# Performance work log

Measured on AMD Instinct MI355X. Metric: run time of the kernel, lower is better.

## Reference

```python
import jax, jax.numpy as jnp
import numpy as np

N, D, H, E = 50000, 128, 256, 400000


def setup_inputs() -> dict:
    key = jax.random.key(0)
    ks = jax.random.split(key, 10)
    s2d = 1.0 / np.sqrt(2 * D)
    sh = 1.0 / np.sqrt(H)
    return {
        "embeddings": jax.random.normal(ks[0], (N, D), jnp.float32),
        "edge_index": jax.random.randint(ks[1], (2, E), 0, N, jnp.int64),
        # contradiction_detector: Linear(2D,H) -> ReLU -> Linear(H,1) -> Sigmoid
        "Wd1": jax.random.uniform(ks[2], (2 * D, H), jnp.float32, -s2d, s2d),
        "bd1": jax.random.uniform(ks[3], (H,), jnp.float32, -s2d, s2d),
        "Wd2": jax.random.uniform(ks[4], (H, 1), jnp.float32, -sh, sh),
        "bd2": jax.random.uniform(ks[5], (1,), jnp.float32, -sh, sh),
        # resolver: Linear(2D,H) -> ReLU -> Linear(H,D)
        "Wr1": jax.random.uniform(ks[6], (2 * D, H), jnp.float32, -s2d, s2d),
        "br1": jax.random.uniform(ks[7], (H,), jnp.float32, -s2d, s2d),
        "Wr2": jax.random.uniform(ks[8], (H, D), jnp.float32, -sh, sh),
        "br2": jax.random.uniform(ks[9], (D,), jnp.float32, -sh, sh),
    }


def reference(embeddings, edge_index, Wd1, bd1, Wd2, bd2, Wr1, br1, Wr2, br2):
    src, dst = edge_index[0], edge_index[1]
    # gather src/dst features for every edge and concat: (E, 2D)
    pair = jnp.concatenate([embeddings[src], embeddings[dst]], axis=-1)
    # batched detector MLP -> per-edge contradiction score (E,)
    scores = jax.nn.sigmoid(jax.nn.relu(pair @ Wd1 + bd1) @ Wd2 + bd2)[:, 0]
    # batched resolver MLP (depends only on ORIGINAL embeddings): (E, D)
    resolution = jax.nn.relu(pair @ Wr1 + br1) @ Wr2 + br2
    mask = scores > 0.5
    n_edges = src.shape[0]
    n_nodes = embeddings.shape[0]
    # Sequential overwrite semantics: the LAST contradicting edge touching a
    order = jnp.where(mask, jnp.arange(1, n_edges + 1, dtype=jnp.int32), 0)
    last = jnp.zeros((n_nodes,), jnp.int32).at[src].max(order).at[dst].max(order)
    idx = jnp.maximum(last - 1, 0)
    resolved = jnp.where((last > 0)[:, None],
                         (embeddings + resolution[idx]) * 0.5,
                         embeddings)
    return resolved, scores
```

## Files before the change

### kernel.cpp

```cpp
#include <hip/hip_runtime.h>
#include <math.h>

#define NN 50000
#define DD 128
#define K2D 256
#define HH 256
#define EE 400000
#define TE 64
#define RT 32
#define PST 260
#define TAU  0.005f
#define TAU2 5e-5f
#define DGRID 512

typedef __attribute__((ext_vector_type(8))) short bf16x8;
typedef __attribute__((ext_vector_type(4))) float f32x4;
typedef unsigned int uint;
typedef unsigned short ushort;

typedef __attribute__((address_space(3))) void lds_void_t;
typedef __attribute__((address_space(1))) void g1_void_t;

__device__ __forceinline__ ushort f2bf(float x) {
    uint u = __builtin_bit_cast(uint, x);
    u = (u + 0x7FFFu + ((u >> 16) & 1u)) >> 16;
    return (ushort)u;
}

__device__ __forceinline__ int stageOff(int r, int k) {
    return ((r >> 4) * 8 + (k >> 5)) * 512 + ((((k >> 3) & 3) << 4) + (r & 15)) * 8 + (k & 7);
}

__device__ __forceinline__ void swz_unit(const float* __restrict__ W,
                                         ushort* __restrict__ out,
                                         int N, int Kt, int unit, int l)
{
    const int n = unit / Kt, t = unit - n * Kt;
    const int row0 = t * 32 + (l >> 4) * 8;
    const int col = n * 16 + (l & 15);
    ushort tmp[8];
#pragma unroll
    for (int j = 0; j < 8; ++j) tmp[j] = f2bf(W[(row0 + j) * N + col]);
    uint4 p;
    p.x = (uint)tmp[0] | ((uint)tmp[1] << 16);
    p.y = (uint)tmp[2] | ((uint)tmp[3] << 16);
    p.z = (uint)tmp[4] | ((uint)tmp[5] << 16);
    p.w = (uint)tmp[6] | ((uint)tmp[7] << 16);
    *(uint4*)(out + ((size_t)unit * 64 + l) * 8) = p;
}

__global__ __launch_bounds__(256) void prep_kernel(
    const float* __restrict__ emb, ushort* __restrict__ embbf, int doConv,
    const float* __restrict__ Wd1, ushort* __restrict__ wd1s,
    const float* __restrict__ Wr1, ushort* __restrict__ wr1s,
    const float* __restrict__ Wr2, ushort* __restrict__ wr2s)
{
    const int gid = blockIdx.x;
    const int tid = threadIdx.x;
    if (gid < 3125) {
        if (!doConv) return;
        const int i = gid * 256 + tid;
        const float4 a = ((const float4*)emb)[(size_t)i * 2];
        const float4 b = ((const float4*)emb)[(size_t)i * 2 + 1];
        uint4 p;
        p.x = (uint)f2bf(a.x) | ((uint)f2bf(a.y) << 16);
        p.y = (uint)f2bf(a.z) | ((uint)f2bf(a.w) << 16);
        p.z = (uint)f2bf(b.x) | ((uint)f2bf(b.y) << 16);
        p.w = (uint)f2bf(b.z) | ((uint)f2bf(b.w) << 16);
        *(uint4*)(embbf + (size_t)i * 8) = p;
        return;
    }
    const int sub = tid >> 6, l = tid & 63;
    if (gid < 3125 + 32) {
        swz_unit(Wd1, wd1s, HH, 8, (gid - 3125) * 4 + sub, l);
    } else if (gid < 3125 + 64) {
        swz_unit(Wr1, wr1s, HH, 8, (gid - 3125 - 32) * 4 + sub, l);
    } else {
        swz_unit(Wr2, wr2s, DD, 8, (gid - 3125 - 64) * 4 + sub, l);
    }
}

__global__ __launch_bounds__(256) void det_pipe(
    const ushort* __restrict__ embbf,
    const int* __restrict__ srcIdx, const int* __restrict__ dstIdx,
    const ushort* __restrict__ w1s, const float* __restrict__ b1,
    const float* __restrict__ W2, const float* __restrict__ b2p,
    float* __restrict__ scores,
    int* __restrict__ last,
    int* __restrict__ flagCount, int* __restrict__ flagList, int flagCap)
{
    __shared__ __align__(16) ushort A[2][TE * K2D];
    __shared__ float zp[2][256];
    const int tid = threadIdx.x;
    const int wv = tid >> 6;
    const int lane = tid & 63;
    const int lc = lane & 15, lg = lane >> 4;
    const int nT = EE / TE;
    const int stride = gridDim.x;

    float b1v[4], w2v[4];
#pragma unroll
    for (int n = 0; n < 4; ++n) {
        const int col = wv * 64 + n * 16 + lc;
        b1v[n] = b1[col];
        w2v[n] = W2[col];
    }
    const float b2v = *b2p;
    const ushort* wbase = w1s + (size_t)(wv * 4) * 8 * 512;

    auto STAGE = [&](int T, int bp) {
        const int e = T * TE + wv * 16 + lc;
        const int ns = srcIdx[e], nd = dstIdx[e];
        const int ko = lg * 8;
#pragma unroll
        for (int s = 0; s < 8; ++s) {
            const int node = (s < 4) ? ns : nd;
            const ushort* g = embbf + (size_t)node * DD + (s & 3) * 32 + ko;
            __builtin_amdgcn_global_load_lds((const g1_void_t*)g,
                                             (lds_void_t*)&A[bp][(wv * 8 + s) * 512],
                                             16, 0, 0);
        }
    };

    int T = blockIdx.x;
    int cur = 0;
    STAGE(T, 0);

    for (; T < nT; T += stride) {
        const int Tn = T + stride;
        if (Tn < nT) {
            STAGE(Tn, cur ^ 1);
            asm volatile("s_waitcnt vmcnt(8)" ::: "memory");
        } else {
            asm volatile("s_waitcnt vmcnt(0)" ::: "memory");
        }
        __builtin_amdgcn_sched_barrier(0);
        __builtin_amdgcn_s_barrier();
        __builtin_amdgcn_sched_barrier(0);

        f32x4 acc[4][4] = {};
#pragma unroll 2
        for (int t = 0; t < 8; ++t) {
            bf16x8 af[4], bfr[4];
#pragma unroll
            for (int m = 0; m < 4; ++m)
                af[m] = *(const bf16x8*)&A[cur][(m * 8 + t) * 512 + lane * 8];
#pragma unroll
            for (int n = 0; n < 4; ++n)
                bfr[n] = *(const bf16x8*)(wbase + (n * 8 + t) * 512 + lane * 8);
#pragma unroll
            for (int m = 0; m < 4; ++m)
#pragma unroll
                for (int n = 0; n < 4; ++n)
                    acc[m][n] = __builtin_amdgcn_mfma_f32_16x16x32_bf16(af[m], bfr[n], acc[m][n], 0, 0, 0);
        }

        float pz[4][4];
#pragma unroll
        for (int m = 0; m < 4; ++m)
#pragma unroll
            for (int r = 0; r < 4; ++r) {
                float s = 0.f;
#pragma unroll
                for (int n = 0; n < 4; ++n)
                    s = fmaf(fmaxf(acc[m][n][r] + b1v[n], 0.f), w2v[n], s);
                pz[m][r] = s;
            }
#pragma unroll
        for (int msk = 1; msk <= 8; msk <<= 1)
#pragma unroll
            for (int m = 0; m < 4; ++m)
#pragma unroll
                for (int r = 0; r < 4; ++r)
                    pz[m][r] += __shfl_xor(pz[m][r], msk, 64);
        if (lc == 0) {
#pragma unroll
            for (int m = 0; m < 4; ++m)
#pragma unroll
                for (int r = 0; r < 4; ++r)
                    zp[cur][wv * 64 + m * 16 + lg * 4 + r] = pz[m][r];
        }

        asm volatile("s_waitcnt lgkmcnt(0)" ::: "memory");
        __builtin_amdgcn_sched_barrier(0);
        __builtin_amdgcn_s_barrier();
        __builtin_amdgcn_sched_barrier(0);

        if (tid < 64) {
            const int e = T * TE + tid;
            const float z = zp[cur][tid] + zp[cur][64 + tid] +
                            zp[cur][128 + tid] + zp[cur][192 + tid] + b2v;
            scores[e] = 1.0f / (1.0f + expf(-z));
            bool deferred = false;
            if (fabsf(z) < TAU) {
                const int slot = atomicAdd(flagCount, 1);
                if (slot < flagCap) { flagList[slot] = e; deferred = true; }
            }
            if (!deferred && z > 0.0f) {
                atomicMax(&last[srcIdx[e]], e + 1);
                atomicMax(&last[dstIdx[e]], e + 1);
            }
        }
        cur ^= 1;
    }
}

__global__ __launch_bounds__(256) void det_kernel(
    const float* __restrict__ emb,
    const int* __restrict__ srcIdx, const int* __restrict__ dstIdx,
    const ushort* __restrict__ w1s, const float* __restrict__ b1,
    const float* __restrict__ W2, const float* __restrict__ b2p,
    float* __restrict__ scores,
    int* __restrict__ last,
    int* __restrict__ flagCount, int* __restrict__ flagList, int flagCap)
{
    __shared__ __align__(16) ushort A_lds[TE * K2D];
    __shared__ float zp[256];
    const int tid = threadIdx.x;
    const int e0 = blockIdx.x * TE;
    {
        const int r = tid >> 2, q = tid & 3;
        const int e = e0 + r;
        const int node = (q < 2) ? srcIdx[e] : dstIdx[e];
        const float4* s4 = (const float4*)(emb + (size_t)node * DD + (q & 1) * 64);
#pragma unroll
        for (int u = 0; u < 16; ++u) {
            const float4 v = s4[u];
            const int k0 = q * 64 + u * 4;
            uint2 p;
            p.x = (uint)f2bf(v.x) | ((uint)f2bf(v.y) << 16);
            p.y = (uint)f2bf(v.z) | ((uint)f2bf(v.w) << 16);
            *(uint2*)&A_lds[stageOff(r, k0)] = p;
        }
    }
    __syncthreads();

    const int wv = tid >> 6;
    const int lane = tid & 63;
    const int lc = lane & 15, lg = lane >> 4;

    f32x4 acc[4][4] = {};
    const ushort* wbase = w1s + (size_t)(wv * 4) * 8 * 512;
#pragma unroll 2
    for (int t = 0; t < 8; ++t) {
        bf16x8 af[4], bfr[4];
#pragma unroll
        for (int m = 0; m < 4; ++m)
            af[m] = *(const bf16x8*)&A_lds[(m * 8 + t) * 512 + lane * 8];
#pragma unroll
        for (int n = 0; n < 4; ++n)
            bfr[n] = *(const bf16x8*)(wbase + (n * 8 + t) * 512 + lane * 8);
#pragma unroll
        for (int m = 0; m < 4; ++m)
#pragma unroll
            for (int n = 0; n < 4; ++n)
                acc[m][n] = __builtin_amdgcn_mfma_f32_16x16x32_bf16(af[m], bfr[n], acc[m][n], 0, 0, 0);
    }
    float b1v[4], w2v[4];
#pragma unroll
    for (int n = 0; n < 4; ++n) {
        const int col = wv * 64 + n * 16 + lc;
        b1v[n] = b1[col];
        w2v[n] = W2[col];
    }
    float pz[4][4];
#pragma unroll
    for (int m = 0; m < 4; ++m)
#pragma unroll
        for (int r = 0; r < 4; ++r) {
            float s = 0.f;
#pragma unroll
            for (int n = 0; n < 4; ++n)
                s = fmaf(fmaxf(acc[m][n][r] + b1v[n], 0.f), w2v[n], s);
            pz[m][r] = s;
        }
#pragma unroll
    for (int msk = 1; msk <= 8; msk <<= 1)
#pragma unroll
        for (int m = 0; m < 4; ++m)
#pragma unroll
            for (int r = 0; r < 4; ++r)
                pz[m][r] += __shfl_xor(pz[m][r], msk, 64);
    if (lc == 0) {
#pragma unroll
        for (int m = 0; m < 4; ++m)
#pragma unroll
            for (int r = 0; r < 4; ++r)
                zp[wv * 64 + m * 16 + lg * 4 + r] = pz[m][r];
    }
    __syncthreads();
    if (tid < 64) {
        const int e = e0 + tid;
        const float z = zp[tid] + zp[64 + tid] + zp[128 + tid] + zp[192 + tid] + *b2p;
        scores[e] = 1.0f / (1.0f + expf(-z));
        bool deferred = false;
        if (fabsf(z) < TAU) {
            const int slot = atomicAdd(flagCount, 1);
            if (slot < flagCap) { flagList[slot] = e; deferred = true; }
        }
        if (!deferred && z > 0.0f) {
            atomicMax(&last[srcIdx[e]], e + 1);
            atomicMax(&last[dstIdx[e]], e + 1);
        }
    }
}

__global__ __launch_bounds__(256) void refine_kernel(
    const float* __restrict__ emb,
    const int* __restrict__ srcIdx, const int* __restrict__ dstIdx,
    const float* __restrict__ W1, const float* __restrict__ b1,
    const float* __restrict__ W2, const float* __restrict__ b2p,
    int* __restrict__ last,
    const int* __restrict__ flagCount, const int* __restrict__ flagList,
    int flagCap)
{
    __shared__ __align__(16) float P[RT * PST];
    __shared__ int eL[RT];
    __shared__ float zs[RT];
    __shared__ int need64[RT];
    __shared__ double wsumd[4];
    const int tid = threadIdx.x;
    const int cnt = min(*flagCount, flagCap);
    const int nTiles = (cnt + RT - 1) / RT;
    const float b2v = *b2p;

    for (int T = blockIdx.x; T < nTiles; T += gridDim.x) {
        if (tid < RT) {
            const int idx = T * RT + tid;
            eL[tid] = flagList[min(idx, cnt - 1)];
            need64[tid] = 0;
        }
        __syncthreads();
        {
            const int i = tid >> 3, q = tid & 7;
            const int e = eL[i];
            const int node = (q < 4) ? srcIdx[e] : dstIdx[e];
            const float4* s4 = (const float4*)(emb + (size_t)node * DD + (q & 3) * 32);
            float4* d4 = (float4*)(P + i * PST + q * 32);
#pragma unroll
            for (int t = 0; t < 8; ++t) d4[t] = s4[t];
        }
        __syncthreads();

        const int rowg = tid >> 5;
        const int colg = tid & 31;
        const int c0 = colg * 8;

        float acc[4][8];
#pragma unroll
        for (int c = 0; c < 8; ++c) {
            const float bv = b1[c0 + c];
#pragma unroll
            for (int r = 0; r < 4; ++r) acc[r][c] = bv;
        }
        for (int kk = 0; kk < K2D; kk += 4) {
            float af[4][4];
#pragma unroll
            for (int r = 0; r < 4; ++r) {
                const float4 v = *(const float4*)&P[(rowg * 4 + r) * PST + kk];
                af[r][0] = v.x; af[r][1] = v.y; af[r][2] = v.z; af[r][3] = v.w;
            }
#pragma unroll
            for (int dk = 0; dk < 4; ++dk) {
                const float4 w0 = *(const float4*)&W1[(kk + dk) * HH + c0];
                const float4 w1 = *(const float4*)&W1[(kk + dk) * HH + c0 + 4];
#pragma unroll
                for (int r = 0; r < 4; ++r) {
                    const float av = af[r][dk];
                    acc[r][0] = fmaf(av, w0.x, acc[r][0]);
                    acc[r][1] = fmaf(av, w0.y, acc[r][1]);
                    acc[r][2] = fmaf(av, w0.z, acc[r][2]);
                    acc[r][3] = fmaf(av, w0.w, acc[r][3]);
                    acc[r][4] = fmaf(av, w1.x, acc[r][4]);
                    acc[r][5] = fmaf(av, w1.y, acc[r][5]);
                    acc[r][6] = fmaf(av, w1.z, acc[r][6]);
                    acc[r][7] = fmaf(av, w1.w, acc[r][7]);
                }
            }
        }

        float w2[8];
#pragma unroll
        for (int c = 0; c < 8; ++c) w2[c] = W2[c0 + c];
        float pz[4];
#pragma unroll
        for (int r = 0; r < 4; ++r) {
            float s = 0.f;
#pragma unroll
            for (int c = 0; c < 8; ++c) s = fmaf(fmaxf(acc[r][c], 0.f), w2[c], s);
            pz[r] = s;
        }
#pragma unroll
        for (int m = 1; m <= 16; m <<= 1) {
#pragma unroll
            for (int r = 0; r < 4; ++r) pz[r] += __shfl_xor(pz[r], m, 64);
        }
        if (colg == 0) {
#pragma unroll
            for (int r = 0; r < 4; ++r) zs[rowg * 4 + r] = pz[r] + b2v;
        }
        __syncthreads();

        if (tid < RT) {
            const int idx = T * RT + tid;
            if (idx < cnt) {
                const float z = zs[tid];
                if (fabsf(z) < TAU2) {
                    need64[tid] = 1;
                } else if (z > 0.f) {
                    const int e = eL[tid];
                    atomicMax(&last[srcIdx[e]], e + 1);
                    atomicMax(&last[dstIdx[e]], e + 1);
                }
            }
        }
        __syncthreads();

        for (int r = 0; r < RT; ++r) {
            if (!need64[r]) continue;
            const int j = tid;
            double h0 = 0.0, h1 = 0.0;
            for (int k = 0; k < K2D; k += 2) {
                h0 += (double)P[r * PST + k]     * (double)W1[(k)     * HH + j];
                h1 += (double)P[r * PST + k + 1] * (double)W1[(k + 1) * HH + j];
            }
            const double h = (double)b1[j] + h0 + h1;
            double v = (h > 0.0) ? h * (double)W2[j] : 0.0;
#pragma unroll
            for (int m = 1; m <= 32; m <<= 1) v += __shfl_xor(v, m, 64);
            if ((tid & 63) == 0) wsumd[tid >> 6] = v;
            __syncthreads();
            if (tid == 0) {
                const double z = wsumd[0] + wsumd[1] + wsumd[2] + wsumd[3] + (double)b2v;
                if (z > 0.0) {
                    const int e = eL[r];
                    atomicMax(&last[srcIdx[e]], e + 1);
                    atomicMax(&last[dstIdx[e]], e + 1);
                }
            }
            __syncthreads();
        }
        __syncthreads();
    }
}

template<int BF>
__global__ __launch_bounds__(256) void res_kernel(
    const float* __restrict__ emb, const ushort* __restrict__ embbf,
    const int* __restrict__ srcIdx, const int* __restrict__ dstIdx,
    const ushort* __restrict__ w1s, const float* __restrict__ b1,
    const ushort* __restrict__ w2s, const float* __restrict__ b2,
    const int* __restrict__ last,
    float* __restrict__ outRes)
{
    __shared__ __align__(16) ushort A_lds[TE * K2D];
    __shared__ int lastL[TE];
    const int tid = threadIdx.x;
    const int n0 = blockIdx.x * TE;
    const int wv = tid >> 6;
    const int lane = tid & 63;

    if (tid < TE) {
        const int n = n0 + tid;
        lastL[tid] = (n < NN) ? last[n] : 0;
    }
    if (BF) {
        const int r = wv * 16 + (lane & 15);
        const int n = n0 + r;
        int e = 0;
        if (n < NN) { const int lv = last[n]; if (lv > 0) e = lv - 1; }
        const int ns = srcIdx[e], nd = dstIdx[e];
        const int ko = (lane >> 4) * 8;
#pragma unroll
        for (int s = 0; s < 8; ++s) {
            const int node = (s < 4) ? ns : nd;
            const ushort* g = embbf + (size_t)node * DD + (s & 3) * 32 + ko;
            __builtin_amdgcn_global_load_lds((const g1_void_t*)g,
                                             (lds_void_t*)&A_lds[(wv * 8 + s) * 512],
                                             16, 0, 0);
        }
    } else {
        const int r = tid >> 2, q = tid & 3;
        const int n = n0 + r;
        int e = 0;
        if (n < NN) { const int l = last[n]; if (l > 0) e = l - 1; }
        const int node = (q < 2) ? srcIdx[e] : dstIdx[e];
        const float4* s4 = (const float4*)(emb + (size_t)node * DD + (q & 1) * 64);
#pragma unroll
        for (int u = 0; u < 16; ++u) {
            const float4 v = s4[u];
            const int k0 = q * 64 + u * 4;
            uint2 p;
            p.x = (uint)f2bf(v.x) | ((uint)f2bf(v.y) << 16);
            p.y = (uint)f2bf(v.z) | ((uint)f2bf(v.w) << 16);
            *(uint2*)&A_lds[stageOff(r, k0)] = p;
        }
    }
    __syncthreads();

    const int lc = lane & 15, lg = lane >> 4;

    f32x4 acc[4][4] = {};
    {
        const ushort* wbase = w1s + (size_t)(wv * 4) * 8 * 512;
#pragma unroll 2
        for (int t = 0; t < 8; ++t) {
            bf16x8 af[4], bfr[4];
#pragma unroll
            for (int m = 0; m < 4; ++m)
                af[m] = *(const bf16x8*)&A_lds[(m * 8 + t) * 512 + lane * 8];
#pragma unroll
            for (int n = 0; n < 4; ++n)
                bfr[n] = *(const bf16x8*)(wbase + (n * 8 + t) * 512 + lane * 8);
#pragma unroll
            for (int m = 0; m < 4; ++m)
#pragma unroll
                for (int n = 0; n < 4; ++n)
                    acc[m][n] = __builtin_amdgcn_mfma_f32_16x16x32_bf16(af[m], bfr[n], acc[m][n], 0, 0, 0);
        }
    }
    float b1v[4];
#pragma unroll
    for (int n = 0; n < 4; ++n) b1v[n] = b1[wv * 64 + n * 16 + lc];

    __syncthreads();
#pragma unroll
    for (int m = 0; m < 4; ++m)
#pragma unroll
        for (int n = 0; n < 4; ++n) {
            const int hcol = wv * 64 + n * 16 + lc;
#pragma unroll
            for (int r = 0; r < 4; ++r) {
                const int row = m * 16 + lg * 4 + r;
                A_lds[stageOff(row, hcol)] = f2bf(fmaxf(acc[m][n][r] + b1v[n], 0.f));
            }
        }
    __syncthreads();

    f32x4 acc2[4][2] = {};
    {
        const ushort* wbase = w2s + (size_t)(wv * 2) * 8 * 512;
#pragma unroll 2
        for (int t = 0; t < 8; ++t) {
            bf16x8 af[4], bfr[2];
#pragma unroll
            for (int m = 0; m < 4; ++m)
                af[m] = *(const bf16x8*)&A_lds[(m * 8 + t) * 512 + lane * 8];
#pragma unroll
            for (int n = 0; n < 2; ++n)
                bfr[n] = *(const bf16x8*)(wbase + (n * 8 + t) * 512 + lane * 8);
#pragma unroll
            for (int m = 0; m < 4; ++m)
#pragma unroll
                for (int n = 0; n < 2; ++n)
                    acc2[m][n] = __builtin_amdgcn_mfma_f32_16x16x32_bf16(af[m], bfr[n], acc2[m][n], 0, 0, 0);
        }
    }
    float b2v[2];
#pragma unroll
    for (int n = 0; n < 2; ++n) b2v[n] = b2[(wv * 2 + n) * 16 + lc];

#pragma unroll
    for (int m = 0; m < 4; ++m)
#pragma unroll
        for (int r = 0; r < 4; ++r) {
            const int row = m * 16 + lg * 4 + r;
            const int n = n0 + row;
            if (n >= NN) continue;
            const bool hit = lastL[row] > 0;
#pragma unroll
            for (int c = 0; c < 2; ++c) {
                const int col = (wv * 2 + c) * 16 + lc;
                const float ev = emb[(size_t)n * DD + col];
                outRes[(size_t)n * DD + col] =
                    hit ? (ev + acc2[m][c][r] + b2v[c]) * 0.5f : ev;
            }
        }
}

extern "C" void kernel_launch(void* const* d_in, const int* in_sizes, int n_in,
                              void* d_out, int out_size, void* d_ws, size_t ws_size,
                              hipStream_t stream)
{
    const float* emb = (const float*)d_in[0];
    const int*   edge = (const int*)d_in[1];
    const float* Wd1 = (const float*)d_in[2];
    const float* bd1 = (const float*)d_in[3];
    const float* Wd2 = (const float*)d_in[4];
    const float* bd2 = (const float*)d_in[5];
    const float* Wr1 = (const float*)d_in[6];
    const float* br1 = (const float*)d_in[7];
    const float* Wr2 = (const float*)d_in[8];
    const float* br2 = (const float*)d_in[9];

    const int* srcIdx = edge;
    const int* dstIdx = edge + EE;

    float* outRes = (float*)d_out;
    float* scores = outRes + (size_t)NN * DD;

    int* last = (int*)d_ws;
    int* flagCount = last + 50112;
    ushort* wd1s = (ushort*)(last + 50176);
    ushort* wr1s = wd1s + 65536;
    ushort* wr2s = wr1s + 65536;
    int* flagList = (int*)(wr2s + 32768);
    ushort* embbf = (ushort*)(flagList + 65536);

    const size_t base   = 50176u * 4 + (65536u + 65536u + 32768u) * 2 + 65536u * 4;
    const size_t needBF = base + (size_t)NN * DD * 2;
    const int useBF = (ws_size >= needBF) ? 1 : 0;

    int flagCap = 65536;
    if (ws_size < base) {
        long avail = ((long)ws_size - (long)(base - 65536u * 4)) / 4;
        flagCap = avail < 0 ? 0 : (int)avail;
    }

    hipMemsetAsync(d_ws, 0, 50176 * sizeof(int), stream);

    prep_kernel<<<3205, 256, 0, stream>>>(emb, embbf, useBF,
                                          Wd1, wd1s, Wr1, wr1s, Wr2, wr2s);

    if (useBF) {
        det_pipe<<<DGRID, 256, 0, stream>>>(embbf, srcIdx, dstIdx,
                                            wd1s, bd1, Wd2, bd2,
                                            scores, last, flagCount, flagList, flagCap);
    } else {
        det_kernel<<<EE / TE, 256, 0, stream>>>(emb, srcIdx, dstIdx,
                                                wd1s, bd1, Wd2, bd2,
                                                scores, last, flagCount, flagList, flagCap);
    }
    refine_kernel<<<1024, 256, 0, stream>>>(emb, srcIdx, dstIdx,
                                            Wd1, bd1, Wd2, bd2,
                                            last, flagCount, flagList, flagCap);
    if (useBF) {
        res_kernel<1><<<(NN + TE - 1) / TE, 256, 0, stream>>>(emb, embbf, srcIdx, dstIdx,
                                                              wr1s, br1, wr2s, br2,
                                                              last, outRes);
    } else {
        res_kernel<0><<<(NN + TE - 1) / TE, 256, 0, stream>>>(emb, embbf, srcIdx, dstIdx,
                                                              wr1s, br1, wr2s, br2,
                                                              last, outRes);
    }
}
```

Baseline: 194.0 us.

## Replace persistent LDS double-buffered detector with one-tile-per-block register-fed kernel

Swaps the persistent, double-buffered detector kernel, which staged gathered bf16 embeddings into LDS with global_load_lds, for a non-persistent kernel launched with one 64-edge tile per block. Each lane loads its A fragments directly from global memory into registers and feeds the MFMAs, so no LDS staging or cross-iteration barriers are needed. A launch_bounds occupancy hint of 3 is added. The intent is to rely on occupancy rather than explicit prefetch to hide gather latency, at the cost of many more block launches and no software pipelining.

```diff
diff --git a/kernel.cpp b/kernel.cpp
--- a/kernel.cpp
+++ b/kernel.cpp
@@ -11,7 +11,6 @@
 #define PST 260
 #define TAU  0.005f
 #define TAU2 5e-5f
-#define DGRID 512
 
 typedef __attribute__((ext_vector_type(8))) short bf16x8;
 typedef __attribute__((ext_vector_type(4))) float f32x4;
@@ -80,7 +79,7 @@
     }
 }
 
-__global__ __launch_bounds__(256) void det_pipe(
+__global__ __launch_bounds__(256, 3) void det_reg(
     const ushort* __restrict__ embbf,
     const int* __restrict__ srcIdx, const int* __restrict__ dstIdx,
     const ushort* __restrict__ w1s, const float* __restrict__ b1,
@@ -89,14 +88,39 @@
     int* __restrict__ last,
     int* __restrict__ flagCount, int* __restrict__ flagList, int flagCap)
 {
-    __shared__ __align__(16) ushort A[2][TE * K2D];
-    __shared__ float zp[2][256];
+    __shared__ float zp[256];
     const int tid = threadIdx.x;
+    const int e0 = blockIdx.x * TE;
     const int wv = tid >> 6;
     const int lane = tid & 63;
     const int lc = lane & 15, lg = lane >> 4;
-    const int nT = EE / TE;
-    const int stride = gridDim.x;
+
+    const ushort* baseS[4];
+    const ushort* baseD[4];
+#pragma unroll
+    for (int m = 0; m < 4; ++m) {
+        const int e = e0 + m * 16 + lc;
+        baseS[m] = embbf + (size_t)srcIdx[e] * DD + lg * 8;
+        baseD[m] = embbf + (size_t)dstIdx[e] * DD + lg * 8;
+    }
+    const ushort* wbase = w1s + (size_t)(wv * 4) * 8 * 512;
+
+    f32x4 acc[4][4] = {};
+#pragma unroll
+    for (int t = 0; t < 8; ++t) {
+        bf16x8 af[4], bfr[4];
+#pragma unroll
+        for (int m = 0; m < 4; ++m)
+            af[m] = *(const bf16x8*)(((t < 4) ? baseS[m] : baseD[m]) + (t & 3) * 32);
+#pragma unroll
+        for (int n = 0; n < 4; ++n)
+            bfr[n] = *(const bf16x8*)(wbase + (size_t)(n * 8 + t) * 512 + lane * 8);
+#pragma unroll
+        for (int m = 0; m < 4; ++m)
+#pragma unroll
+            for (int n = 0; n < 4; ++n)
+                acc[m][n] = __builtin_amdgcn_mfma_f32_16x16x32_bf16(af[m], bfr[n], acc[m][n], 0, 0, 0);
+    }
 
     float b1v[4], w2v[4];
 #pragma unroll
@@ -105,103 +129,46 @@
         b1v[n] = b1[col];
         w2v[n] = W2[col];
     }
-    const float b2v = *b2p;
-    const ushort* wbase = w1s + (size_t)(wv * 4) * 8 * 512;
-
-    auto STAGE = [&](int T, int bp) {
-        const int e = T * TE + wv * 16 + lc;
-        const int ns = srcIdx[e], nd = dstIdx[e];
-        const int ko = lg * 8;
-#pragma unroll
-        for (int s = 0; s < 8; ++s) {
-            const int node = (s < 4) ? ns : nd;
-            const ushort* g = embbf + (size_t)node * DD + (s & 3) * 32 + ko;
-            __builtin_amdgcn_global_load_lds((const g1_void_t*)g,
-                                             (lds_void_t*)&A[bp][(wv * 8 + s) * 512],
-                                             16, 0, 0);
-        }
-    };
-
-    int T = blockIdx.x;
-    int cur = 0;
-    STAGE(T, 0);
-
-    for (; T < nT; T += stride) {
-        const int Tn = T + stride;
-        if (Tn < nT) {
-            STAGE(Tn, cur ^ 1);
-            asm volatile("s_waitcnt vmcnt(8)" ::: "memory");
-        } else {
-            asm volatile("s_waitcnt vmcnt(0)" ::: "memory");
-        }
-        __builtin_amdgcn_sched_barrier(0);
-        __builtin_amdgcn_s_barrier();
-        __builtin_amdgcn_sched_barrier(0);
-
-        f32x4 acc[4][4] = {};
-#pragma unroll 2
-        for (int t = 0; t < 8; ++t) {
-            bf16x8 af[4], bfr[4];
-#pragma unroll
-            for (int m = 0; m < 4; ++m)
-                af[m] = *(const bf16x8*)&A[cur][(m * 8 + t) * 512 + lane * 8];
+    float pz[4][4];
+#pragma unroll
+    for (int m = 0; m < 4; ++m)
+#pragma unroll
+        for (int r = 0; r < 4; ++r) {
+            float s = 0.f;
 #pragma unroll
             for (int n = 0; n < 4; ++n)
-                bfr[n] = *(const bf16x8*)(wbase + (n * 8 + t) * 512 + lane * 8);
-#pragma unroll
-            for (int m = 0; m < 4; ++m)
-#pragma unroll
-                for (int n = 0; n < 4; ++n)
-                    acc[m][n] = __builtin_amdgcn_mfma_f32_16x16x32_bf16(af[m], bfr[n], acc[m][n], 0, 0, 0);
-        }
-
-        float pz[4][4];
-#pragma unroll
-        for (int m = 0; m < 4; ++m)
-#pragma unroll
-            for (int r = 0; r < 4; ++r) {
-                float s = 0.f;
-#pragma unroll
-                for (int n = 0; n < 4; ++n)
-                    s = fmaf(fmaxf(acc[m][n][r] + b1v[n], 0.f), w2v[n], s);
-                pz[m][r] = s;
-            }
-#pragma unroll
-        for (int msk = 1; msk <= 8; msk <<= 1)
-#pragma unroll
-            for (int m = 0; m < 4; ++m)
-#pragma unroll
-                for (int r = 0; r < 4; ++r)
-                    pz[m][r] += __shfl_xor(pz[m][r], msk, 64);
-        if (lc == 0) {
-#pragma unroll
-            for (int m = 0; m < 4; ++m)
-#pragma unroll
-                for (int r = 0; r < 4; ++r)
-                    zp[cur][wv * 64 + m * 16 + lg * 4 + r] = pz[m][r];
-        }
-
-        asm volatile("s_waitcnt lgkmcnt(0)" ::: "memory");
-        __builtin_amdgcn_sched_barrier(0);
-        __builtin_amdgcn_s_barrier();
-        __builtin_amdgcn_sched_barrier(0);
-
-        if (tid < 64) {
-            const int e = T * TE + tid;
-            const float z = zp[cur][tid] + zp[cur][64 + tid] +
-                            zp[cur][128 + tid] + zp[cur][192 + tid] + b2v;
-            scores[e] = 1.0f / (1.0f + expf(-z));
-            bool deferred = false;
-            if (fabsf(z) < TAU) {
-                const int slot = atomicAdd(flagCount, 1);
-                if (slot < flagCap) { flagList[slot] = e; deferred = true; }
-            }
-            if (!deferred && z > 0.0f) {
-                atomicMax(&last[srcIdx[e]], e + 1);
-                atomicMax(&last[dstIdx[e]], e + 1);
-            }
-        }
-        cur ^= 1;
+                s = fmaf(fmaxf(acc[m][n][r] + b1v[n], 0.f), w2v[n], s);
+            pz[m][r] = s;
+        }
+#pragma unroll
+    for (int msk = 1; msk <= 8; msk <<= 1)
+#pragma unroll
+        for (int m = 0; m < 4; ++m)
+#pragma unroll
+            for (int r = 0; r < 4; ++r)
+                pz[m][r] += __shfl_xor(pz[m][r], msk, 64);
+    if (lc == 0) {
+#pragma unroll
+        for (int m = 0; m < 4; ++m)
+#pragma unroll
+            for (int r = 0; r < 4; ++r)
+                zp[wv * 64 + m * 16 + lg * 4 + r] = pz[m][r];
+    }
+    __syncthreads();
+
+    if (tid < 64) {
+        const int e = e0 + tid;
+        const float z = zp[tid] + zp[64 + tid] + zp[128 + tid] + zp[192 + tid] + *b2p;
+        scores[e] = 1.0f / (1.0f + expf(-z));
+        bool deferred = false;
+        if (fabsf(z) < TAU) {
+            const int slot = atomicAdd(flagCount, 1);
+            if (slot < flagCap) { flagList[slot] = e; deferred = true; }
+        }
+        if (!deferred && z > 0.0f) {
+            atomicMax(&last[srcIdx[e]], e + 1);
+            atomicMax(&last[dstIdx[e]], e + 1);
+        }
     }
 }
 
@@ -623,9 +590,9 @@
                                           Wd1, wd1s, Wr1, wr1s, Wr2, wr2s);
 
     if (useBF) {
-        det_pipe<<<DGRID, 256, 0, stream>>>(embbf, srcIdx, dstIdx,
-                                            wd1s, bd1, Wd2, bd2,
-                                            scores, last, flagCount, flagList, flagCap);
+        det_reg<<<EE / TE, 256, 0, stream>>>(embbf, srcIdx, dstIdx,
+                                             wd1s, bd1, Wd2, bd2,
+                                             scores, last, flagCount, flagList, flagCap);
     } else {
         det_kernel<<<EE / TE, 256, 0, stream>>>(emb, srcIdx, dstIdx,
                                                 wd1s, bd1, Wd2, bd2,
```

Measured after the change: 251.5 us. 1.3x slower.

## Halve detector edge tile to 32 and double grid size

Applied to the files above, without the earlier changes.

The detector pipeline kernel now processes 32 edges per tile instead of 64, halving the LDS staging buffer and the accumulator registers per wave, and the grid is doubled to 1024 blocks. Staging is redistributed so each wave loads one side (src or dst) for 16 edges, and the epilogue spreads the final reduction across four waves. The intent is higher occupancy and better latency hiding for the gathered loads, at the cost of reloading the W1 fragments for half as many MFMAs per load.

```diff
diff --git a/kernel.cpp b/kernel.cpp
--- a/kernel.cpp
+++ b/kernel.cpp
@@ -7,11 +7,12 @@
 #define HH 256
 #define EE 400000
 #define TE 64
+#define TD 32
 #define RT 32
 #define PST 260
 #define TAU  0.005f
 #define TAU2 5e-5f
-#define DGRID 512
+#define DGRID 1024
 
 typedef __attribute__((ext_vector_type(8))) short bf16x8;
 typedef __attribute__((ext_vector_type(4))) float f32x4;
@@ -89,13 +90,13 @@
     int* __restrict__ last,
     int* __restrict__ flagCount, int* __restrict__ flagList, int flagCap)
 {
-    __shared__ __align__(16) ushort A[2][TE * K2D];
-    __shared__ float zp[2][256];
+    __shared__ __align__(16) ushort A[2][TD * K2D];
+    __shared__ float zp[2][4][TD];
     const int tid = threadIdx.x;
     const int wv = tid >> 6;
     const int lane = tid & 63;
     const int lc = lane & 15, lg = lane >> 4;
-    const int nT = EE / TE;
+    const int nT = EE / TD;
     const int stride = gridDim.x;
 
     float b1v[4], w2v[4];
@@ -108,29 +109,28 @@
     const float b2v = *b2p;
     const ushort* wbase = w1s + (size_t)(wv * 4) * 8 * 512;
 
+    const int sm = wv >> 1, shalf = wv & 1;
     auto STAGE = [&](int T, int bp) {
-        const int e = T * TE + wv * 16 + lc;
-        const int ns = srcIdx[e], nd = dstIdx[e];
-        const int ko = lg * 8;
-#pragma unroll
-        for (int s = 0; s < 8; ++s) {
-            const int node = (s < 4) ? ns : nd;
-            const ushort* g = embbf + (size_t)node * DD + (s & 3) * 32 + ko;
-            __builtin_amdgcn_global_load_lds((const g1_void_t*)g,
-                                             (lds_void_t*)&A[bp][(wv * 8 + s) * 512],
+        const int e = T * TD + sm * 16 + lc;
+        const int node = shalf ? dstIdx[e] : srcIdx[e];
+        const ushort* gb = embbf + (size_t)node * DD + lg * 8;
+#pragma unroll
+        for (int s = 0; s < 4; ++s)
+            __builtin_amdgcn_global_load_lds((const g1_void_t*)(gb + s * 32),
+                                             (lds_void_t*)&A[bp][(wv * 4 + s) * 512],
                                              16, 0, 0);
-        }
     };
 
     int T = blockIdx.x;
     int cur = 0;
+    if (T >= nT) return;
     STAGE(T, 0);
 
     for (; T < nT; T += stride) {
         const int Tn = T + stride;
         if (Tn < nT) {
             STAGE(Tn, cur ^ 1);
-            asm volatile("s_waitcnt vmcnt(8)" ::: "memory");
+            asm volatile("s_waitcnt vmcnt(4)" ::: "memory");
         } else {
             asm volatile("s_waitcnt vmcnt(0)" ::: "memory");
         }
@@ -138,47 +138,39 @@
         __builtin_amdgcn_s_barrier();
         __builtin_amdgcn_sched_barrier(0);
 
-        f32x4 acc[4][4] = {};
-#pragma unroll 2
+        f32x4 acc[2][4] = {};
+#pragma unroll
         for (int t = 0; t < 8; ++t) {
-            bf16x8 af[4], bfr[4];
-#pragma unroll
-            for (int m = 0; m < 4; ++m)
-                af[m] = *(const bf16x8*)&A[cur][(m * 8 + t) * 512 + lane * 8];
-#pragma unroll
-            for (int n = 0; n < 4; ++n)
-                bfr[n] = *(const bf16x8*)(wbase + (n * 8 + t) * 512 + lane * 8);
-#pragma unroll
-            for (int m = 0; m < 4; ++m)
-#pragma unroll
-                for (int n = 0; n < 4; ++n)
-                    acc[m][n] = __builtin_amdgcn_mfma_f32_16x16x32_bf16(af[m], bfr[n], acc[m][n], 0, 0, 0);
-        }
-
-        float pz[4][4];
-#pragma unroll
-        for (int m = 0; m < 4; ++m)
+            const bf16x8 a0 = *(const bf16x8*)&A[cur][(0 * 8 + t) * 512 + lane * 8];
+            const bf16x8 a1 = *(const bf16x8*)&A[cur][(1 * 8 + t) * 512 + lane * 8];
+#pragma unroll
+            for (int n = 0; n < 4; ++n) {
+                acc[0][n] = __builtin_amdgcn_mfma_f32_16x16x32_bf16(a0, *(const bf16x8*)(wbase + (size_t)(n * 8 + t) * 512 + lane * 8), acc[0][n], 0, 0, 0);
+                acc[1][n] = __builtin_amdgcn_mfma_f32_16x16x32_bf16(a1, *(const bf16x8*)(wbase + (size_t)(n * 8 + t) * 512 + lane * 8), acc[1][n], 0, 0, 0);
+            }
+        }
+
+#pragma unroll
+        for (int mm = 0; mm < 2; ++mm) {
+            float pz[4];
 #pragma unroll
             for (int r = 0; r < 4; ++r) {
                 float s = 0.f;
 #pragma unroll
                 for (int n = 0; n < 4; ++n)
-                    s = fmaf(fmaxf(acc[m][n][r] + b1v[n], 0.f), w2v[n], s);
-                pz[m][r] = s;
-            }
-#pragma unroll
-        for (int msk = 1; msk <= 8; msk <<= 1)
-#pragma unroll
-            for (int m = 0; m < 4; ++m)
+                    s = fmaf(fmaxf(acc[mm][n][r] + b1v[n], 0.f), w2v[n], s);
+                pz[r] = s;
+            }
+#pragma unroll
+            for (int msk = 1; msk <= 8; msk <<= 1)
 #pragma unroll
                 for (int r = 0; r < 4; ++r)
-                    pz[m][r] += __shfl_xor(pz[m][r], msk, 64);
-        if (lc == 0) {
-#pragma unroll
-            for (int m = 0; m < 4; ++m)
+                    pz[r] += __shfl_xor(pz[r], msk, 64);
+            if (lc == 0) {
 #pragma unroll
                 for (int r = 0; r < 4; ++r)
-                    zp[cur][wv * 64 + m * 16 + lg * 4 + r] = pz[m][r];
+                    zp[cur][wv][mm * 16 + lg * 4 + r] = pz[r];
+            }
         }
 
         asm volatile("s_waitcnt lgkmcnt(0)" ::: "memory");
@@ -186,10 +178,11 @@
         __builtin_amdgcn_s_barrier();
         __builtin_amdgcn_sched_barrier(0);
 
-        if (tid < 64) {
-            const int e = T * TE + tid;
-            const float z = zp[cur][tid] + zp[cur][64 + tid] +
-                            zp[cur][128 + tid] + zp[cur][192 + tid] + b2v;
+        if (lane < 8) {
+            const int row = wv * 8 + lane;
+            const int e = T * TD + row;
+            const float z = zp[cur][0][row] + zp[cur][1][row] +
+                            zp[cur][2][row] + zp[cur][3][row] + b2v;
             scores[e] = 1.0f / (1.0f + expf(-z));
             bool deferred = false;
             if (fabsf(z) < TAU) {
```

Result: slower. 254.9 us (+31.4%).
